# Performance work log

Hardware: AMD Instinct MI355X
Metric: run time of the kernel (lower is better)

## Reference

```python
import jax, jax.numpy as jnp
import numpy as np

N_IN = 1000000   # non-empty input octants at depth d
N_OUT = 125000   # parent octants at depth d-1 (stride-2 downsample)
C_IN = 96
C_OUT = 192
K = 8            # 2x2x2 kernel -> 8 children per parent
BN_EPS = 1e-5


def setup_inputs() -> dict:
    key = jax.random.key(0)
    k1, k2, k3, k4 = jax.random.split(key, 4)
    data = jax.random.normal(k1, (N_IN, C_IN), dtype=jnp.float32)
    # child-neighbor table: index into input rows; <0 would mean empty child
    neigh = jax.random.randint(k2, (N_OUT, K), 0, N_IN, dtype=jnp.int64)
    # OctreeConv weights [K, Cin, Cout] + bias, BatchNorm affine params
    fan_in = K * C_IN
    weights = jax.random.normal(k3, (K, C_IN, C_OUT), dtype=jnp.float32) / np.sqrt(fan_in)
    bias = jax.random.normal(k4, (C_OUT,), dtype=jnp.float32) * 0.01
    gamma = jnp.ones((C_OUT,), dtype=jnp.float32)
    beta = jnp.zeros((C_OUT,), dtype=jnp.float32)
    return {"data": data, "weights": weights, "bias": bias,
            "gamma": gamma, "beta": beta, "neigh": neigh}


def reference(data, weights, bias, gamma, beta, neigh):
    # --- OctreeConv, kernel 2x2x2, stride 2, nempty=True ---
    valid = neigh >= 0                                   # [M, K]
    idx = jnp.clip(neigh, 0)                             # safe gather index
    gathered = data[idx]                                 # [M, K, Cin]
    gathered = jnp.where(valid[:, :, None], gathered, 0.0)
    out = jnp.einsum('mkc,kcd->md', gathered, weights) + bias  # [M, Cout]
    # --- BatchNorm1d over node dim (training-mode batch stats) ---
    mean = jnp.mean(out, axis=0)
    var = jnp.var(out, axis=0)                           # biased variance
    out = (out - mean) * jax.lax.rsqrt(var + BN_EPS) * gamma + beta
    return out
```

## Files before the change

### kernel.cpp

```cpp
#include <hip/hip_runtime.h>

#define M_OUT   125000
#define CIN     96
#define COUT    192
#define KOCT    8
#define MT      256
#define LDA     104
#define LDB     104
#define BN_EPS  1e-5f

#define WS_SCALE_OFF 384
#define WS_WT_BYTE   4096

typedef __attribute__((ext_vector_type(8))) short bf16x8;
typedef __attribute__((ext_vector_type(4))) float f32x4;

__device__ __forceinline__ unsigned short f2bf(float f) {
    unsigned int u = __float_as_uint(f);
    u += 0x7FFF + ((u >> 16) & 1);
    return (unsigned short)(u >> 16);
}

__device__ __forceinline__ unsigned int pack2(float a, float b) {
    unsigned int ua = __float_as_uint(a);
    unsigned int ub = __float_as_uint(b);
    ua += 0x7FFF + ((ua >> 16) & 1);
    ub += 0x7FFF + ((ub >> 16) & 1);
    return (ua >> 16) | (ub & 0xFFFF0000u);
}

__device__ __forceinline__ bf16x8 pack8(const float4 h0, const float4 h1) {
    union { unsigned int u[4]; bf16x8 v; } r;
    r.u[0] = pack2(h0.x, h0.y);
    r.u[1] = pack2(h0.z, h0.w);
    r.u[2] = pack2(h1.x, h1.y);
    r.u[3] = pack2(h1.z, h1.w);
    return r.v;
}

__device__ __forceinline__ int sel8(const int4 a, const int4 b, int k) {
    switch (k & 7) {
        case 0: return a.x; case 1: return a.y; case 2: return a.z; case 3: return a.w;
        case 4: return b.x; case 5: return b.y; case 6: return b.z; default: return b.w;
    }
}

__global__ void prep_kernel(const float* __restrict__ W, float* __restrict__ ws_f,
                            unsigned short* __restrict__ wt) {
    int gid = blockIdx.x * blockDim.x + threadIdx.x;
    if (gid < 384) ws_f[gid] = 0.0f;
    if (gid < KOCT * COUT * LDA) {
        int c = gid % LDA;
        int rest = gid / LDA;
        int n = rest % COUT;
        int k = rest / COUT;
        float v = (c < CIN) ? W[(k * CIN + c) * COUT + n] : 0.0f;
        wt[gid] = f2bf(v);
    }
}

__global__ __launch_bounds__(512, 2)
void conv_kernel(const float* __restrict__ data,
                 const int* __restrict__ neigh,
                 const float* __restrict__ bias,
                 const unsigned short* __restrict__ wt,
                 float* __restrict__ out,
                 float* __restrict__ gsum) {
    __shared__ __align__(16) unsigned short Bs[2][COUT * LDB];
    __shared__ float stats[2 * COUT];

    const int t    = threadIdx.x;
    const int wave = t >> 6;
    const int lane = t & 63;
    const int quad = lane >> 4;
    const int l15  = lane & 15;
    const int m0   = blockIdx.x * MT;

    for (int i = t; i < 2 * COUT; i += 512) stats[i] = 0.0f;

    int4 nid[2][2];
#pragma unroll
    for (int rt = 0; rt < 2; ++rt) {
        int gm = m0 + wave * 32 + rt * 16 + l15;
        if (gm < M_OUT) {
            nid[rt][0] = *reinterpret_cast<const int4*>(neigh + (size_t)gm * 8);
            nid[rt][1] = *reinterpret_cast<const int4*>(neigh + (size_t)gm * 8 + 4);
        } else {
            nid[rt][0] = make_int4(-1, -1, -1, -1);
            nid[rt][1] = make_int4(-1, -1, -1, -1);
        }
    }

    f32x4 acc[2][12];
    const f32x4 vz = {0.f, 0.f, 0.f, 0.f};
#pragma unroll
    for (int i = 0; i < 2; ++i)
#pragma unroll
        for (int j = 0; j < 12; ++j) acc[i][j] = vz;

    float4 ar[12];
    bf16x8 af[2][2][3];

    auto gather = [&](int k) {
#pragma unroll
        for (int rt = 0; rt < 2; ++rt) {
            int idx = sel8(nid[rt][0], nid[rt][1], k);
            const float* p = data + (size_t)idx * CIN + quad * 8;
#pragma unroll
            for (int ks = 0; ks < 3; ++ks)
#pragma unroll
                for (int h = 0; h < 2; ++h) {
                    float4 v = {0.f, 0.f, 0.f, 0.f};
                    if (idx >= 0) v = *reinterpret_cast<const float4*>(p + ks * 32 + h * 4);
                    ar[(rt * 3 + ks) * 2 + h] = v;
                }
        }
    };
    auto packA = [&](int buf) {
#pragma unroll
        for (int rt = 0; rt < 2; ++rt)
#pragma unroll
            for (int ks = 0; ks < 3; ++ks)
                af[buf][rt][ks] = pack8(ar[(rt * 3 + ks) * 2], ar[(rt * 3 + ks) * 2 + 1]);
    };
    auto stageB = [&](int k, int buf) {
        const char* src = (const char*)wt + (size_t)k * (COUT * LDB * 2);
        char* dst = (char*)&Bs[buf][0];
#pragma unroll
        for (int j = 0; j < 5; ++j) {
            int chunk = wave + 8 * j;
            if (chunk < 39) {
                __builtin_amdgcn_global_load_lds(
                    (const __attribute__((address_space(1))) unsigned int*)(src + chunk * 1024 + lane * 16),
                    (__attribute__((address_space(3))) unsigned int*)(dst + chunk * 1024 + lane * 16),
                    16, 0, 0);
            }
        }
    };
    auto mfmaPhase = [&](int kbuf, int bbuf) {
#pragma unroll
        for (int ks = 0; ks < 3; ++ks)
#pragma unroll
            for (int h = 0; h < 2; ++h) {
                bf16x8 bfr[6];
#pragma unroll
                for (int c = 0; c < 6; ++c) {
                    int n = h * 96 + c * 16 + l15;
                    bfr[c] = *reinterpret_cast<const bf16x8*>(&Bs[bbuf][n * LDB + ks * 32 + quad * 8]);
                }
#pragma unroll
                for (int rt = 0; rt < 2; ++rt)
#pragma unroll
                    for (int c = 0; c < 6; ++c)
                        acc[rt][h * 6 + c] = __builtin_amdgcn_mfma_f32_16x16x32_bf16(
                            af[kbuf][rt][ks], bfr[c], acc[rt][h * 6 + c], 0, 0, 0);
            }
    };

    gather(0);
    stageB(0, 0);
    packA(0);
    __syncthreads();

#pragma unroll
    for (int k = 0; k < KOCT; ++k) {
        const int cb = k & 1;
        if (k < KOCT - 1) {
            gather(k + 1);
            stageB(k + 1, cb ^ 1);
        }
        __builtin_amdgcn_sched_barrier(0);
        mfmaPhase(cb, cb);
        __builtin_amdgcn_sched_barrier(0);
        if (k < KOCT - 1) packA(cb ^ 1);
        __syncthreads();
    }

#pragma unroll
    for (int ct = 0; ct < 12; ++ct) {
        int col = ct * 16 + l15;
        float b = bias[col];
        float s1 = 0.f, s2 = 0.f;
#pragma unroll
        for (int rt = 0; rt < 2; ++rt) {
#pragma unroll
            for (int r = 0; r < 4; ++r) {
                int gm = m0 + wave * 32 + rt * 16 + quad * 4 + r;
                if (gm < M_OUT) {
                    float v = acc[rt][ct][r] + b;
                    out[(size_t)gm * COUT + col] = v;
                    s1 += v;
                    s2 += v * v;
                }
            }
        }
        s1 += __shfl_xor(s1, 16); s2 += __shfl_xor(s2, 16);
        s1 += __shfl_xor(s1, 32); s2 += __shfl_xor(s2, 32);
        if (quad == 0) {
            atomicAdd(&stats[col], s1);
            atomicAdd(&stats[COUT + col], s2);
        }
    }
    __syncthreads();
    for (int i = t; i < COUT; i += 512) {
        atomicAdd(&gsum[i], stats[i]);
        atomicAdd(&gsum[COUT + i], stats[COUT + i]);
    }
}

__global__ void finalize_kernel(const float* __restrict__ gsum,
                                const float* __restrict__ gamma,
                                const float* __restrict__ beta,
                                float* __restrict__ ss) {
    int c = threadIdx.x;
    if (c < COUT) {
        float inv_m = 1.0f / (float)M_OUT;
        float mean = gsum[c] * inv_m;
        float var  = gsum[COUT + c] * inv_m - mean * mean;
        float rstd = rsqrtf(var + BN_EPS);
        float sc   = gamma[c] * rstd;
        ss[c]        = sc;
        ss[COUT + c] = beta[c] - mean * sc;
    }
}

__global__ void norm_kernel(float* __restrict__ out, const float* __restrict__ ss) {
    __shared__ float s_scale[COUT], s_shift[COUT];
    for (int i = threadIdx.x; i < COUT; i += blockDim.x) {
        s_scale[i] = ss[i];
        s_shift[i] = ss[COUT + i];
    }
    __syncthreads();
    const int total4 = M_OUT * COUT / 4;
    int stride = gridDim.x * blockDim.x;
    for (int i = blockIdx.x * blockDim.x + threadIdx.x; i < total4; i += stride) {
        float4 v = reinterpret_cast<float4*>(out)[i];
        int c4 = (i % (COUT / 4)) * 4;
        v.x = v.x * s_scale[c4 + 0] + s_shift[c4 + 0];
        v.y = v.y * s_scale[c4 + 1] + s_shift[c4 + 1];
        v.z = v.z * s_scale[c4 + 2] + s_shift[c4 + 2];
        v.w = v.w * s_scale[c4 + 3] + s_shift[c4 + 3];
        reinterpret_cast<float4*>(out)[i] = v;
    }
}

extern "C" void kernel_launch(void* const* d_in, const int* in_sizes, int n_in,
                              void* d_out, int out_size, void* d_ws, size_t ws_size,
                              hipStream_t stream) {
    const float* data  = (const float*)d_in[0];
    const float* W     = (const float*)d_in[1];
    const float* bias  = (const float*)d_in[2];
    const float* gamma = (const float*)d_in[3];
    const float* beta  = (const float*)d_in[4];
    const int*   neigh = (const int*)d_in[5];
    float* out  = (float*)d_out;
    float* ws_f = (float*)d_ws;
    unsigned short* wt = (unsigned short*)((char*)d_ws + WS_WT_BYTE);

    prep_kernel<<<(KOCT * COUT * LDA + 255) / 256, 256, 0, stream>>>(W, ws_f, wt);

    int grid1 = (M_OUT + MT - 1) / MT;
    conv_kernel<<<grid1, 512, 0, stream>>>(data, neigh, bias, wt, out, ws_f);

    finalize_kernel<<<1, 192, 0, stream>>>(ws_f, gamma, beta, ws_f + WS_SCALE_OFF);

    norm_kernel<<<4096, 256, 0, stream>>>(out, ws_f + WS_SCALE_OFF);
}
```

Baseline: 595.6 us.

## Drop LDS weight staging, split columns across waves, fold finalize into norm

The conv kernel no longer stages bf16 weights through shared memory with per-step block barriers. Each wave now reads its B fragments straight from global memory (L2-resident) and covers half of the output columns for 32 rows, so the block tile shrinks to 128 rows. The A gather is double-buffered two steps ahead to hide load latency. The finalize kernel is merged into the norm kernel, which saves one launch. In exchange, weights are read redundantly from global/L2 by every wave, each gathered row is loaded twice (once per column-half wave), and register pressure rises.

```diff
diff --git a/kernel.cpp b/kernel.cpp
--- a/kernel.cpp
+++ b/kernel.cpp
@@ -4,12 +4,10 @@
 #define CIN     96
 #define COUT    192
 #define KOCT    8
-#define MT      256
-#define LDA     104
+#define MT      128
 #define LDB     104
 #define BN_EPS  1e-5f
 
-#define WS_SCALE_OFF 384
 #define WS_WT_BYTE   4096
 
 typedef __attribute__((ext_vector_type(8))) short bf16x8;
@@ -49,9 +47,9 @@
                             unsigned short* __restrict__ wt) {
     int gid = blockIdx.x * blockDim.x + threadIdx.x;
     if (gid < 384) ws_f[gid] = 0.0f;
-    if (gid < KOCT * COUT * LDA) {
-        int c = gid % LDA;
-        int rest = gid / LDA;
+    if (gid < KOCT * COUT * LDB) {
+        int c = gid % LDB;
+        int rest = gid / LDB;
         int n = rest % COUT;
         int k = rest / COUT;
         float v = (c < CIN) ? W[(k * CIN + c) * COUT + n] : 0.0f;
@@ -66,7 +64,6 @@
                  const unsigned short* __restrict__ wt,
                  float* __restrict__ out,
                  float* __restrict__ gsum) {
-    __shared__ __align__(16) unsigned short Bs[2][COUT * LDB];
     __shared__ float stats[2 * COUT];
 
     const int t    = threadIdx.x;
@@ -74,14 +71,18 @@
     const int lane = t & 63;
     const int quad = lane >> 4;
     const int l15  = lane & 15;
+    const int rg   = wave >> 1;
+    const int ch   = wave & 1;
     const int m0   = blockIdx.x * MT;
+    const int row0 = m0 + rg * 32;
 
     for (int i = t; i < 2 * COUT; i += 512) stats[i] = 0.0f;
+    __syncthreads();
 
     int4 nid[2][2];
 #pragma unroll
     for (int rt = 0; rt < 2; ++rt) {
-        int gm = m0 + wave * 32 + rt * 16 + l15;
+        int gm = row0 + rt * 16 + l15;
         if (gm < M_OUT) {
             nid[rt][0] = *reinterpret_cast<const int4*>(neigh + (size_t)gm * 8);
             nid[rt][1] = *reinterpret_cast<const int4*>(neigh + (size_t)gm * 8 + 4);
@@ -91,20 +92,20 @@
         }
     }
 
-    f32x4 acc[2][12];
+    f32x4 acc[2][6];
     const f32x4 vz = {0.f, 0.f, 0.f, 0.f};
 #pragma unroll
     for (int i = 0; i < 2; ++i)
 #pragma unroll
-        for (int j = 0; j < 12; ++j) acc[i][j] = vz;
-
-    float4 ar[12];
-    bf16x8 af[2][2][3];
-
-    auto gather = [&](int k) {
+        for (int j = 0; j < 6; ++j) acc[i][j] = vz;
+
+    float4 arA[12], arB[12];
+    bf16x8 af[2][3];
+
+    auto gather = [&](float4 (&AR)[12], int K) {
 #pragma unroll
         for (int rt = 0; rt < 2; ++rt) {
-            int idx = sel8(nid[rt][0], nid[rt][1], k);
+            int idx = sel8(nid[rt][0], nid[rt][1], K);
             const float* p = data + (size_t)idx * CIN + quad * 8;
 #pragma unroll
             for (int ks = 0; ks < 3; ++ks)
@@ -112,80 +113,63 @@
                 for (int h = 0; h < 2; ++h) {
                     float4 v = {0.f, 0.f, 0.f, 0.f};
                     if (idx >= 0) v = *reinterpret_cast<const float4*>(p + ks * 32 + h * 4);
-                    ar[(rt * 3 + ks) * 2 + h] = v;
+                    AR[(rt * 3 + ks) * 2 + h] = v;
                 }
         }
     };
-    auto packA = [&](int buf) {
+    auto packA = [&](float4 (&AR)[12]) {
 #pragma unroll
         for (int rt = 0; rt < 2; ++rt)
 #pragma unroll
             for (int ks = 0; ks < 3; ++ks)
-                af[buf][rt][ks] = pack8(ar[(rt * 3 + ks) * 2], ar[(rt * 3 + ks) * 2 + 1]);
-    };
-    auto stageB = [&](int k, int buf) {
-        const char* src = (const char*)wt + (size_t)k * (COUT * LDB * 2);
-        char* dst = (char*)&Bs[buf][0];
-#pragma unroll
-        for (int j = 0; j < 5; ++j) {
-            int chunk = wave + 8 * j;
-            if (chunk < 39) {
-                __builtin_amdgcn_global_load_lds(
-                    (const __attribute__((address_space(1))) unsigned int*)(src + chunk * 1024 + lane * 16),
-                    (__attribute__((address_space(3))) unsigned int*)(dst + chunk * 1024 + lane * 16),
-                    16, 0, 0);
-            }
-        }
-    };
-    auto mfmaPhase = [&](int kbuf, int bbuf) {
-#pragma unroll
-        for (int ks = 0; ks < 3; ++ks)
-#pragma unroll
-            for (int h = 0; h < 2; ++h) {
-                bf16x8 bfr[6];
-#pragma unroll
-                for (int c = 0; c < 6; ++c) {
-                    int n = h * 96 + c * 16 + l15;
-                    bfr[c] = *reinterpret_cast<const bf16x8*>(&Bs[bbuf][n * LDB + ks * 32 + quad * 8]);
-                }
-#pragma unroll
-                for (int rt = 0; rt < 2; ++rt)
-#pragma unroll
-                    for (int c = 0; c < 6; ++c)
-                        acc[rt][h * 6 + c] = __builtin_amdgcn_mfma_f32_16x16x32_bf16(
-                            af[kbuf][rt][ks], bfr[c], acc[rt][h * 6 + c], 0, 0, 0);
-            }
-    };
-
-    gather(0);
-    stageB(0, 0);
-    packA(0);
-    __syncthreads();
-
+                af[rt][ks] = pack8(AR[(rt * 3 + ks) * 2], AR[(rt * 3 + ks) * 2 + 1]);
+    };
+    auto loadB = [&](bf16x8 (&BF)[6], int K, int KS) {
+#pragma unroll
+        for (int c = 0; c < 6; ++c) {
+            int n = ch * 96 + c * 16 + l15;
+            BF[c] = *reinterpret_cast<const bf16x8*>(
+                wt + ((size_t)K * COUT + n) * LDB + KS * 32 + quad * 8);
+        }
+    };
+    auto mfmaG = [&](bf16x8 (&BF)[6], int KS) {
+#pragma unroll
+        for (int rt = 0; rt < 2; ++rt)
+#pragma unroll
+            for (int c = 0; c < 6; ++c)
+                acc[rt][c] = __builtin_amdgcn_mfma_f32_16x16x32_bf16(
+                    af[rt][KS], BF[c], acc[rt][c], 0, 0, 0);
+    };
+
+    gather(arA, 0);
+    gather(arB, 1);
+
+    bf16x8 b0[6], b1[6];
 #pragma unroll
     for (int k = 0; k < KOCT; ++k) {
-        const int cb = k & 1;
-        if (k < KOCT - 1) {
-            gather(k + 1);
-            stageB(k + 1, cb ^ 1);
-        }
+        loadB(b0, k, 0);
+        if (k & 1) packA(arB); else packA(arA);
+        if (k < KOCT - 2) {
+            if (k & 1) gather(arB, k + 2); else gather(arA, k + 2);
+        }
+        loadB(b1, k, 1);
         __builtin_amdgcn_sched_barrier(0);
-        mfmaPhase(cb, cb);
-        __builtin_amdgcn_sched_barrier(0);
-        if (k < KOCT - 1) packA(cb ^ 1);
-        __syncthreads();
-    }
-
-#pragma unroll
-    for (int ct = 0; ct < 12; ++ct) {
-        int col = ct * 16 + l15;
+        mfmaG(b0, 0);
+        loadB(b0, k, 2);
+        mfmaG(b1, 1);
+        mfmaG(b0, 2);
+    }
+
+#pragma unroll
+    for (int ct = 0; ct < 6; ++ct) {
+        int col = ch * 96 + ct * 16 + l15;
         float b = bias[col];
         float s1 = 0.f, s2 = 0.f;
 #pragma unroll
         for (int rt = 0; rt < 2; ++rt) {
 #pragma unroll
             for (int r = 0; r < 4; ++r) {
-                int gm = m0 + wave * 32 + rt * 16 + quad * 4 + r;
+                int gm = row0 + rt * 16 + quad * 4 + r;
                 if (gm < M_OUT) {
                     float v = acc[rt][ct][r] + b;
                     out[(size_t)gm * COUT + col] = v;
@@ -208,27 +192,18 @@
     }
 }
 
-__global__ void finalize_kernel(const float* __restrict__ gsum,
-                                const float* __restrict__ gamma,
-                                const float* __restrict__ beta,
-                                float* __restrict__ ss) {
-    int c = threadIdx.x;
-    if (c < COUT) {
-        float inv_m = 1.0f / (float)M_OUT;
-        float mean = gsum[c] * inv_m;
-        float var  = gsum[COUT + c] * inv_m - mean * mean;
-        float rstd = rsqrtf(var + BN_EPS);
-        float sc   = gamma[c] * rstd;
-        ss[c]        = sc;
-        ss[COUT + c] = beta[c] - mean * sc;
-    }
-}
-
-__global__ void norm_kernel(float* __restrict__ out, const float* __restrict__ ss) {
+__global__ void norm_kernel(float* __restrict__ out,
+                            const float* __restrict__ gsum,
+                            const float* __restrict__ gamma,
+                            const float* __restrict__ beta) {
     __shared__ float s_scale[COUT], s_shift[COUT];
     for (int i = threadIdx.x; i < COUT; i += blockDim.x) {
-        s_scale[i] = ss[i];
-        s_shift[i] = ss[COUT + i];
+        const float inv_m = 1.0f / (float)M_OUT;
+        float mean = gsum[i] * inv_m;
+        float var  = gsum[COUT + i] * inv_m - mean * mean;
+        float sc   = gamma[i] * rsqrtf(var + BN_EPS);
+        s_scale[i] = sc;
+        s_shift[i] = beta[i] - mean * sc;
     }
     __syncthreads();
     const int total4 = M_OUT * COUT / 4;
@@ -257,12 +232,10 @@
     float* ws_f = (float*)d_ws;
     unsigned short* wt = (unsigned short*)((char*)d_ws + WS_WT_BYTE);
 
-    prep_kernel<<<(KOCT * COUT * LDA + 255) / 256, 256, 0, stream>>>(W, ws_f, wt);
+    prep_kernel<<<(KOCT * COUT * LDB + 255) / 256, 256, 0, stream>>>(W, ws_f, wt);
 
     int grid1 = (M_OUT + MT - 1) / MT;
     conv_kernel<<<grid1, 512, 0, stream>>>(data, neigh, bias, wt, out, ws_f);
 
-    finalize_kernel<<<1, 192, 0, stream>>>(ws_f, gamma, beta, ws_f + WS_SCALE_OFF);
-
-    norm_kernel<<<4096, 256, 0, stream>>>(out, ws_f + WS_SCALE_OFF);
-}
+    norm_kernel<<<4096, 256, 0, stream>>>(out, ws_f, gamma, beta);
+}
```

Result: slower. 720.3 us (+20.9%).
